# Performance work log

Hardware: AMD Instinct MI355X
Metric: run time of the kernel (lower is better)

The kernel has to match this reference:

```python
import jax, jax.numpy as jnp
import numpy as np

LMAX, MMAX = 4, 2
L1 = LMAX + 1                      # 5 coefficients with m=0
NL = [LMAX + 1 - m for m in range(MMAX + 1)]   # [5,4,3] degrees per |m|
K = (LMAX + 1) ** 2                # 25 full SH coefficients
KR = NL[0] + 2 * sum(NL[1:])       # 19 coefficients with |m|<=mmax
# degree l of each row in the reduced (m-primary) layout:
# m=0: l=0..4 | m=+1: l=1..4 | m=-1: l=1..4 | m=+2: l=2..4 | m=-2: l=2..4
L_IDX = np.array([0,1,2,3,4, 1,2,3,4, 1,2,3,4, 2,3,4, 2,3,4])


def so2_conv(x, rad, w0, b0, wr1, wi1, wr2, wi2, c_out, extra):
    """SO(2)-equivariant conv over m-primary layout x: [E, KR, c_in].
    rad: optional per-edge radial weights [E, sum_m nl_m*c_in]."""
    E, _, c_in = x.shape
    # m = 0 block
    x0 = x[:, :L1].reshape(E, L1 * c_in)
    if rad is not None:
        x0 = x0 * rad[:, :L1 * c_in]
    y0 = x0 @ w0 + b0
    out0 = y0[:, :L1 * c_out].reshape(E, L1, c_out)
    gating = y0[:, L1 * c_out:] if extra else None
    outs = [out0]
    off_x, off_r = L1, L1 * c_in
    for nl, wr, wi in ((NL[1], wr1, wi1), (NL[2], wr2, wi2)):
        xr = x[:, off_x:off_x + nl].reshape(E, nl * c_in)
        xi = x[:, off_x + nl:off_x + 2 * nl].reshape(E, nl * c_in)
        if rad is not None:
            rm = rad[:, off_r:off_r + nl * c_in]
            xr, xi = xr * rm, xi * rm
        yr = xr @ wr - xi @ wi   # complex-style SO2 mixing
        yi = xi @ wr + xr @ wi
        outs += [yr.reshape(E, nl, c_out), yi.reshape(E, nl, c_out)]
        off_x += 2 * nl
        off_r += nl * c_in
    return jnp.concatenate(outs, axis=1), gating


def gate_act(gating, x):
    """GateActivation: silu on l=0 scalars, sigmoid gates per degree l>=1."""
    E, _, H = x.shape
    g = jax.nn.sigmoid(gating).reshape(E, LMAX, H)
    g_ext = jnp.concatenate([jnp.ones((E, 1, H), x.dtype), g], axis=1)
    out = x * g_ext[:, L_IDX]           # l=0 row gated by 1, replaced below
    return out.at[:, 0].set(jax.nn.silu(x[:, 0]))


def setup_inputs() -> dict:
    key = jax.random.key(0)
    ks = jax.random.split(key, 32)
    E, N, C, H, D, RH = 50000, 2500, 64, 64, 128, 64
    c_in1 = 2 * C
    rad_dim = sum(nl * c_in1 for nl in NL)          # 1536
    extra = LMAX * H                                 # 256

    def w(k, shape):
        return jax.random.normal(k, shape, jnp.float32) / np.sqrt(shape[0])

    inp = {
        'node_feats': jax.random.normal(ks[0], (N, K, C), jnp.float32),
        'edge_embeds': jax.random.normal(ks[1], (E, D), jnp.float32),
        'wigner': jax.random.normal(ks[2], (E, KR, K), jnp.float32) / np.sqrt(K),
        'wigner_inv': jax.random.normal(ks[3], (E, K, KR), jnp.float32) / np.sqrt(KR),
        'edge_envelope': jax.random.uniform(ks[4], (E, 1, 1), jnp.float32),
        'rad_w1': w(ks[5], (D, RH)), 'rad_b1': jnp.zeros((RH,), jnp.float32),
        'rad_w2': w(ks[6], (RH, rad_dim)), 'rad_b2': jnp.zeros((rad_dim,), jnp.float32),
        'w1_m0': w(ks[7], (L1 * c_in1, L1 * H + extra)),
        'b1_m0': jnp.zeros((L1 * H + extra,), jnp.float32),
        'w1_r1': w(ks[8], (NL[1] * c_in1, NL[1] * H)),
        'w1_i1': w(ks[9], (NL[1] * c_in1, NL[1] * H)),
        'w1_r2': w(ks[10], (NL[2] * c_in1, NL[2] * H)),
        'w1_i2': w(ks[11], (NL[2] * c_in1, NL[2] * H)),
        'w2_m0': w(ks[12], (L1 * H, L1 * C)),
        'b2_m0': jnp.zeros((L1 * C,), jnp.float32),
        'w2_r1': w(ks[13], (NL[1] * H, NL[1] * C)),
        'w2_i1': w(ks[14], (NL[1] * H, NL[1] * C)),
        'w2_r2': w(ks[15], (NL[2] * H, NL[2] * C)),
        'w2_i2': w(ks[16], (NL[2] * H, NL[2] * C)),
        'senders': jax.random.randint(ks[17], (E,), 0, N, jnp.int32),
        'receivers': jax.random.randint(ks[18], (E,), 0, N, jnp.int32),
    }
    return inp


def reference(node_feats, edge_embeds, wigner, wigner_inv, edge_envelope,
              rad_w1, rad_b1, rad_w2, rad_b2,
              w1_m0, b1_m0, w1_r1, w1_i1, w1_r2, w1_i2,
              w2_m0, b2_m0, w2_r1, w2_i1, w2_r2, w2_i2,
              senders, receivers):
    num_nodes = node_feats.shape[0]
    C = node_feats.shape[2]
    H = w2_m0.shape[0] // L1
    # gather + concat: [E, K, 2C]
    msg = jnp.concatenate((node_feats[senders], node_feats[receivers]), axis=2)
    # rotate to edge frame, truncated to |m|<=mmax: [E, KR, 2C]
    msg = jnp.einsum('erk,ekc->erc', wigner, msg)
    # per-edge radial weights for conv1
    rad = jax.nn.silu(edge_embeds @ rad_w1 + rad_b1) @ rad_w2 + rad_b2
    msg, gating = so2_conv(msg, rad, w1_m0, b1_m0, w1_r1, w1_i1, w1_r2, w1_i2,
                           c_out=H, extra=LMAX * H)
    msg = gate_act(gating, msg)
    msg, _ = so2_conv(msg, None, w2_m0, b2_m0, w2_r1, w2_i1, w2_r2, w2_i2,
                      c_out=C, extra=0)
    msg = msg * edge_envelope
    # rotate back to global frame: [E, K, C]
    msg = jnp.einsum('ekr,erc->ekc', wigner_inv, msg)
    return jax.ops.segment_sum(msg, receivers, num_segments=num_nodes)
```

## Files before the change

### kernel.cpp

```cpp
#include <hip/hip_runtime.h>


typedef __attribute__((ext_vector_type(8))) short bf16x8;
typedef __attribute__((ext_vector_type(4))) float f32x4;

union U8 { uint4 v; unsigned short s[8]; };

__device__ __forceinline__ unsigned short f2b(float f) {
    unsigned u = __float_as_uint(f);
    unsigned r = (u + 0x7FFFu + ((u >> 16) & 1u)) >> 16;
    return (unsigned short)r;
}
__device__ __forceinline__ float b2f(unsigned short h) {
    return __uint_as_float(((unsigned)h) << 16);
}
__device__ __forceinline__ float sigm_(float x){ return 1.0f/(1.0f+__expf(-x)); }
__device__ __forceinline__ float silu_(float x){ return x/(1.0f+__expf(-x)); }

__device__ __forceinline__ void async16(short* lds, const short* g) {
    __builtin_amdgcn_global_load_lds(
        (const __attribute__((address_space(1))) void*)g,
        (__attribute__((address_space(3))) void*)lds, 16, 0, 0);
}

#define OFF_W1T   0L
#define OFF_W1C1  409600L
#define OFF_W1C2  933888L
#define OFF_V0T   1327104L
#define OFF_V1C   1449984L
#define OFF_V2C   1712128L
#define OFF_RW2T  1908736L
#define W_TOTAL   2007040L
#define NNODES    2500
#define NFT_ELEMS (2500L * 2048L)

__global__ void k_prep(const float* __restrict__ w1m0, const float* __restrict__ w1r1,
                       const float* __restrict__ w1i1, const float* __restrict__ w1r2,
                       const float* __restrict__ w1i2, const float* __restrict__ w2m0,
                       const float* __restrict__ w2r1, const float* __restrict__ w2i1,
                       const float* __restrict__ w2r2, const float* __restrict__ w2i2,
                       const float* __restrict__ rw2, short* __restrict__ W)
{
    long i = (long)blockIdx.x * blockDim.x + threadIdx.x;
    if (i >= W_TOTAL) return;
    float v;
    if (i < OFF_W1C1) {
        int n = (int)(i / 640), k = (int)(i % 640);
        v = (n < 576) ? w1m0[k * 576 + n] : 0.f;
    } else if (i < OFF_W1C2) {
        long j = i - OFF_W1C1; int n = (int)(j >> 10), k = (int)(j & 1023);
        v = (n < 256) ? ((k < 512) ? w1r1[k*256 + n] : -w1i1[(k-512)*256 + n])
                      : ((k < 512) ? w1i1[k*256 + (n-256)] : w1r1[(k-512)*256 + (n-256)]);
    } else if (i < OFF_V0T) {
        long j = i - OFF_W1C2; int n = (int)(j / 768), k = (int)(j % 768);
        v = (n >= 384) ? 0.f
          : (n < 192) ? ((k < 384) ? w1r2[k*192 + n] : -w1i2[(k-384)*192 + n])
                      : ((k < 384) ? w1i2[k*192 + (n-192)] : w1r2[(k-384)*192 + (n-192)]);
    } else if (i < OFF_V1C) {
        long j = i - OFF_V0T; int n = (int)(j / 320), k = (int)(j % 320);
        v = (n < 320) ? w2m0[k * 320 + n] : 0.f;
    } else if (i < OFF_V2C) {
        long j = i - OFF_V1C; int n = (int)(j >> 9), k = (int)(j & 511);
        v = (n < 256) ? ((k < 256) ? w2r1[k*256 + n] : -w2i1[(k-256)*256 + n])
                      : ((k < 256) ? w2i1[k*256 + (n-256)] : w2r1[(k-256)*256 + (n-256)]);
    } else if (i < OFF_RW2T) {
        long j = i - OFF_V2C; int n = (int)(j / 384), k = (int)(j % 384);
        v = (n >= 384) ? 0.f
          : (n < 192) ? ((k < 192) ? w2r2[k*192 + n] : -w2i2[(k-192)*192 + n])
                      : ((k < 192) ? w2i2[k*192 + (n-192)] : w2r2[(k-192)*192 + (n-192)]);
    } else {
        long j = i - OFF_RW2T; int n = (int)(j >> 6), d = (int)(j & 63);
        v = rw2[d * 1536 + n];
    }
    W[i] = (short)f2b(v);
}

__global__ __launch_bounds__(256)
void k_nft(const float* __restrict__ nf, short* __restrict__ nfT)
{
    __shared__ float s_nf[25 * 65];
    const int t = threadIdx.x;
    const long nn = blockIdx.x;
    for (int p = t; p < 1600; p += 256) {
        int r = p >> 6, c = p & 63;
        s_nf[r * 65 + c] = nf[nn * 1600 + p];
    }
    __syncthreads();
    for (int i = t; i < 2048; i += 256) {
        int c = i >> 5, k = i & 31;
        float v = (k < 25) ? s_nf[k * 65 + c] : 0.f;
        nfT[nn * 2048 + i] = (short)f2b(v);
    }
}

__global__ void k_hist(const int* __restrict__ rcv, int* __restrict__ cnt, long e0, long n)
{
    long e = (long)blockIdx.x * 256 + threadIdx.x;
    if (e < n) atomicAdd(&cnt[rcv[e0 + e]], 1);
}

__global__ __launch_bounds__(256)
void k_scan(const int* __restrict__ cnt, int* __restrict__ off, int* __restrict__ nxt)
{
    __shared__ int part[256];
    const int t = threadIdx.x;
    const int base = t * 10;
    int loc[10]; int s = 0;
    #pragma unroll
    for (int j = 0; j < 10; ++j) {
        int idx = base + j;
        int v = (idx < NNODES) ? cnt[idx] : 0;
        loc[j] = s; s += v;
    }
    part[t] = s;
    __syncthreads();
    for (int d = 1; d < 256; d <<= 1) {
        int v = part[t];
        int u = (t >= d) ? part[t - d] : 0;
        __syncthreads();
        part[t] = v + u;
        __syncthreads();
    }
    int excl = (t == 0) ? 0 : part[t - 1];
    #pragma unroll
    for (int j = 0; j < 10; ++j) {
        int idx = base + j;
        if (idx < NNODES) { int o = excl + loc[j]; off[idx] = o; nxt[idx] = o; }
    }
}

__global__ void k_scat(const int* __restrict__ rcv, int* __restrict__ nxt,
                       int* __restrict__ perm, long e0, long n)
{
    long e = (long)blockIdx.x * 256 + threadIdx.x;
    if (e < n) {
        int p = atomicAdd(&nxt[rcv[e0 + e]], 1);
        perm[p] = (int)e;
    }
}

__global__ __launch_bounds__(512)
void k_rad(const float* __restrict__ ee, const float* __restrict__ rw1,
           const float* __restrict__ rb1, const float* __restrict__ rb2,
           const short* __restrict__ RW2T, short* __restrict__ rad,
           long e0, long Etot)
{
    __shared__ __align__(16) short s_h[32 * 64];
    const int t = threadIdx.x, w = t >> 6, l = t & 63, l15 = l & 15, lhi = l >> 4;
    const long eb = (long)blockIdx.x * 32;

    #pragma unroll
    for (int j = 0; j < 4; ++j) {
        int i = t + j * 512;
        int e = i >> 6, d = i & 63;
        long ge = e0 + eb + e;
        float a = rb1[d];
        if (ge < Etot) {
            const float* ep = ee + ge * 128;
            #pragma unroll 16
            for (int dd = 0; dd < 128; ++dd) a = fmaf(ep[dd], rw1[dd * 64 + d], a);
            a = silu_(a);
        } else a = 0.f;
        *(short*)((char*)s_h + e * 128 + ((d * 2) ^ ((e & 7) << 4))) = (short)f2b(a);
    }
    __syncthreads();

    f32x4 acc[6][2][2];
    #pragma unroll
    for (int g = 0; g < 6; ++g)
        #pragma unroll
        for (int mt = 0; mt < 2; ++mt)
            #pragma unroll
            for (int nt = 0; nt < 2; ++nt)
                acc[g][mt][nt] = (f32x4){0.f, 0.f, 0.f, 0.f};

    #pragma unroll
    for (int ks = 0; ks < 2; ++ks) {
        bf16x8 af[2];
        #pragma unroll
        for (int mt = 0; mt < 2; ++mt)
            af[mt] = *(const bf16x8*)((const char*)s_h + (mt * 16 + l15) * 128 +
                                      (((ks << 6) + (lhi << 4)) ^ ((l & 7) << 4)));
        #pragma unroll
        for (int g = 0; g < 6; ++g) {
            int grp = w + g * 8;
            #pragma unroll
            for (int nt = 0; nt < 2; ++nt) {
                int col = grp * 32 + nt * 16 + l15;
                bf16x8 bf = *(const bf16x8*)(RW2T + (long)col * 64 + (ks << 5) + (lhi << 3));
                #pragma unroll
                for (int mt = 0; mt < 2; ++mt)
                    acc[g][mt][nt] = __builtin_amdgcn_mfma_f32_16x16x32_bf16(af[mt], bf, acc[g][mt][nt], 0, 0, 0);
            }
        }
    }
    #pragma unroll
    for (int g = 0; g < 6; ++g)
        #pragma unroll
        for (int nt = 0; nt < 2; ++nt) {
            int col = (w + g * 8) * 32 + nt * 16 + l15;
            float bias = rb2[col];
            #pragma unroll
            for (int mt = 0; mt < 2; ++mt)
                #pragma unroll
                for (int r = 0; r < 4; ++r) {
                    int e = mt * 16 + lhi * 4 + r;
                    rad[(eb + e) * 1536 + col] = (short)f2b(acc[g][mt][nt][r] + bias);
                }
        }
}

__global__ __launch_bounds__(256)
void k_rot2(const float* __restrict__ wig, const short* __restrict__ nfT,
            const short* __restrict__ rad,
            const int* __restrict__ snd, const int* __restrict__ rcv,
            short* __restrict__ X, long e0, long nchunk)
{
    __shared__ float s_wg[4][480];
    __shared__ __align__(16) short s_rot[4][20 * 128];
    const int t = threadIdx.x, w = t >> 6, l = t & 63, l15 = l & 15, lhi = l >> 4;
    const long eb = (long)blockIdx.x * 4;
    const long el = eb + w;
    const bool valid = (el < nchunk);

    for (int p = t; p < 4 * 475; p += 256) {
        int e = p / 475, q = p - e * 475;
        if (eb + e < nchunk) s_wg[e][q] = wig[(e0 + eb + e) * 475 + q];
    }
    __syncthreads();

    if (valid) {
        long ge = e0 + el;
        int n0 = snd[ge], n1 = rcv[ge];
        U8 a0u, a1u;
        #pragma unroll
        for (int j = 0; j < 8; ++j) {
            int k = lhi * 8 + j;
            a0u.s[j] = (k < 25) ? f2b(s_wg[w][l15 * 25 + k]) : (unsigned short)0;
            a1u.s[j] = (l15 < 3 && k < 25) ? f2b(s_wg[w][(16 + l15) * 25 + k]) : (unsigned short)0;
        }
        bf16x8 a0 = *(bf16x8*)&a0u, a1 = *(bf16x8*)&a1u;

        f32x4 acc0[8], acc1[8];
        #pragma unroll
        for (int nt = 0; nt < 8; ++nt) {
            acc0[nt] = (f32x4){0.f, 0.f, 0.f, 0.f};
            acc1[nt] = (f32x4){0.f, 0.f, 0.f, 0.f};
        }
        #pragma unroll
        for (int nt = 0; nt < 8; ++nt) {
            int col = nt * 16 + l15;
            bf16x8 b = *(const bf16x8*)(nfT + (long)(col < 64 ? n0 : n1) * 2048 +
                                        (long)(col & 63) * 32 + (lhi << 3));
            acc0[nt] = __builtin_amdgcn_mfma_f32_16x16x32_bf16(a0, b, acc0[nt], 0, 0, 0);
            acc1[nt] = __builtin_amdgcn_mfma_f32_16x16x32_bf16(a1, b, acc1[nt], 0, 0, 0);
        }
        char* base = (char*)s_rot[w];
        #pragma unroll
        for (int nt = 0; nt < 8; ++nt) {
            int col2 = (nt * 16 + l15) * 2;
            #pragma unroll
            for (int r = 0; r < 4; ++r) {
                int row = lhi * 4 + r;
                *(short*)(base + ((row * 256 + col2) ^ ((row & 7) << 4))) = (short)f2b(acc0[nt][r]);
            }
            if (lhi == 0) {
                #pragma unroll
                for (int r = 0; r < 4; ++r) {
                    int row = 16 + r;
                    *(short*)(base + ((row * 256 + col2) ^ ((row & 7) << 4))) = (short)f2b(acc1[nt][r]);
                }
            }
        }
    }
    __syncthreads();

    short* xp = X + el * 2432;
    if (valid) {
        const short* rp = rad + el * 1536;
        #pragma unroll
        for (int it = 0; it < 5; ++it) {
            int q = l + it * 64;
            if (q < 304) {
                int r = q >> 4, c0 = (q & 15) << 3;
                int rr = (r < 9) ? r : ((r < 16) ? r - 4 : r - 7);
                U8 rot; rot.v = *(uint4*)((char*)s_rot[w] + ((r * 256 + c0 * 2) ^ ((r & 7) << 4)));
                U8 rd;  rd.v  = *(const uint4*)(rp + rr * 128 + c0);
                U8 o;
                #pragma unroll
                for (int j = 0; j < 8; ++j) o.s[j] = f2b(b2f(rot.s[j]) * b2f(rd.s[j]));
                *(uint4*)(xp + q * 8) = o.v;
            }
        }
    } else {
        #pragma unroll
        for (int it = 0; it < 5; ++it) {
            int q = l + it * 64;
            if (q < 304) *(uint4*)(xp + q * 8) = (uint4){0, 0, 0, 0};
        }
    }
}

__global__ __launch_bounds__(256)
void k_gate(short* __restrict__ Zr, long nitems)
{
    long idx = (long)blockIdx.x * 256 + threadIdx.x;
    if (idx >= nitems) return;
    long e = idx / 152;
    int jg = (int)(idx - e * 152);
    int j = jg * 8;
    short* rp = Zr + e * 1536;
    U8 z; z.v = *(const uint4*)(rp + j);
    U8 o;
    if (j < 320) {
        int rr = j >> 6;
        if (rr == 0) {
            #pragma unroll
            for (int q = 0; q < 8; ++q) o.s[q] = f2b(silu_(b2f(z.s[q])));
        } else {
            U8 g; g.v = *(const uint4*)(rp + 1216 + (rr - 1) * 64 + (j & 63));
            #pragma unroll
            for (int q = 0; q < 8; ++q) o.s[q] = f2b(b2f(z.s[q]) * b2f(g.s[q]));
        }
    } else if (j < 832) {
        U8 g; g.v = *(const uint4*)(rp + 1216 + ((j - 320) & 255));
        #pragma unroll
        for (int q = 0; q < 8; ++q) o.s[q] = f2b(b2f(z.s[q]) * b2f(g.s[q]));
    } else {
        int gi = j - 832; if (gi >= 192) gi -= 192;
        U8 g; g.v = *(const uint4*)(rp + 1280 + gi);
        #pragma unroll
        for (int q = 0; q < 8; ++q) o.s[q] = f2b(b2f(z.s[q]) * b2f(g.s[q]));
    }
    *(uint4*)(rp + j) = o.v;
}

template<int Km, int Nreal, int EPI>
__device__ __forceinline__ void gemm_body(
    const short* __restrict__ A, const long RS,
    const short* __restrict__ W, const float* __restrict__ bias,
    short* __restrict__ O, const long OS, const int oofs,
    short* __restrict__ sA, short* __restrict__ sB, const int et, const int cb)
{
    const int t = threadIdx.x, w = t >> 6, l = t & 63, l15 = l & 15, lhi = l >> 4;
    const int wm = w & 1, wn = w >> 1;
    const long eb = (long)et * 128;
    const short* Ap = A + eb * RS;
    const short* Wp = W + (long)cb * Km;

    f32x4 acc[4][4];
    #pragma unroll
    for (int mt = 0; mt < 4; ++mt)
        #pragma unroll
        for (int nt = 0; nt < 4; ++nt)
            acc[mt][nt] = (f32x4){0.f, 0.f, 0.f, 0.f};

    int rowA[2], k8A[2];
    #pragma unroll
    for (int i = 0; i < 2; ++i) {
        int s = i * 512 + t;
        rowA[i] = s >> 3;
        k8A[i]  = (s & 7) ^ (rowA[i] & 7);
    }
    int rowB[4], k8B[4];
    #pragma unroll
    for (int i = 0; i < 4; ++i) {
        int s = i * 512 + t;
        rowB[i] = s >> 3;
        k8B[i]  = (s & 7) ^ (rowB[i] & 7);
    }
    const int wb = w << 6;

    const int rx = l & 7;
    constexpr int NCH = Km / 64;
    for (int ch = 0; ch < NCH; ++ch) {
        const int kc = ch * 64;
        __syncthreads();
        #pragma unroll
        for (int i = 0; i < 2; ++i)
            async16(sA + (i * 512 + wb) * 8, Ap + (long)rowA[i] * RS + kc + k8A[i] * 8);
        #pragma unroll
        for (int i = 0; i < 4; ++i)
            async16(sB + (i * 512 + wb) * 8, Wp + (long)rowB[i] * Km + kc + k8B[i] * 8);
        __syncthreads();
        #pragma unroll
        for (int ks = 0; ks < 2; ++ks) {
            const int ko = (((ks << 2) + lhi) ^ rx) << 3;
            bf16x8 af[4], bf[4];
            #pragma unroll
            for (int mt = 0; mt < 4; ++mt) {
                int row = wm * 64 + mt * 16 + l15;
                af[mt] = *(const bf16x8*)(sA + row * 64 + ko);
            }
            #pragma unroll
            for (int nt = 0; nt < 4; ++nt) {
                int row = wn * 64 + nt * 16 + l15;
                bf[nt] = *(const bf16x8*)(sB + row * 64 + ko);
            }
            #pragma unroll
            for (int mt = 0; mt < 4; ++mt)
                #pragma unroll
                for (int nt = 0; nt < 4; ++nt)
                    acc[mt][nt] = __builtin_amdgcn_mfma_f32_16x16x32_bf16(af[mt], bf[nt], acc[mt][nt], 0, 0, 0);
        }
    }

    const int r0 = wm * 64, c0 = wn * 64;
    #pragma unroll
    for (int nt = 0; nt < 4; ++nt) {
        int jj = cb + c0 + nt * 16 + l15;
        if (jj < Nreal) {
            float b = (EPI >= 1) ? bias[jj] : 0.f;
            #pragma unroll
            for (int mt = 0; mt < 4; ++mt)
                #pragma unroll
                for (int r = 0; r < 4; ++r) {
                    long e = eb + r0 + mt * 16 + lhi * 4 + r;
                    float v = acc[mt][nt][r] + b;
                    if constexpr (EPI == 2) {
                        if (jj < 320) O[e * OS + jj] = (short)f2b(v);
                        else          O[e * OS + 1216 + (jj - 320)] = (short)f2b(sigm_(v));
                    } else {
                        O[e * OS + oofs + jj] = (short)f2b(v);
                    }
                }
        }
    }
}

__global__ __launch_bounds__(512)
void k_conv1(const short* __restrict__ X, const short* __restrict__ W0,
             const short* __restrict__ W1, const short* __restrict__ W2,
             const float* __restrict__ b1m0, short* __restrict__ Zr, int nbt)
{
    __shared__ __align__(16) short sA[8192];
    __shared__ __align__(16) short sB[16384];
    const int bid = blockIdx.x;
    const int s = bid >> 3;
    const int et = (bid & 7) + ((s / 7) << 3);
    const int ph = s % 7;
    if (et >= nbt) return;
    if (ph < 3)
        gemm_body< 640, 576, 2>(X,        2432, W0, b1m0,   Zr, 1536, 0,   sA, sB, et, ph << 8);
    else if (ph < 5)
        gemm_body<1024, 512, 0>(X + 640,  2432, W1, nullptr, Zr, 1536, 320, sA, sB, et, (ph - 3) << 8);
    else
        gemm_body< 768, 384, 0>(X + 1664, 2432, W2, nullptr, Zr, 1536, 832, sA, sB, et, (ph - 5) << 8);
}

__global__ __launch_bounds__(512)
void k_conv2(const short* __restrict__ Zr, const short* __restrict__ V0,
             const short* __restrict__ V1, const short* __restrict__ V2,
             const float* __restrict__ b2m0, short* __restrict__ Y2, int nbt)
{
    __shared__ __align__(16) short sA[8192];
    __shared__ __align__(16) short sB[16384];
    const int bid = blockIdx.x;
    const int s = bid >> 3;
    const int et = (bid & 7) + ((s / 6) << 3);
    const int ph = s % 6;
    if (et >= nbt) return;
    if (ph < 2)
        gemm_body<320, 320, 1>(Zr,       1536, V0, b2m0,   Y2, 1216, 0,   sA, sB, et, ph << 8);
    else if (ph < 4)
        gemm_body<512, 512, 0>(Zr + 320, 1536, V1, nullptr, Y2, 1216, 320, sA, sB, et, (ph - 2) << 8);
    else
        gemm_body<384, 384, 0>(Zr + 832, 1536, V2, nullptr, Y2, 1216, 832, sA, sB, et, (ph - 4) << 8);
}

__global__ __launch_bounds__(256)
void k_invn(const short* __restrict__ Y2, const float* __restrict__ winv,
            const float* __restrict__ env, const int* __restrict__ cnt,
            const int* __restrict__ off, const int* __restrict__ perm,
            float* __restrict__ out, long e0)
{
    __shared__ __align__(16) short s_y[2][1216];
    __shared__ float s_wv[2][476];
    const int t = threadIdx.x;
    const int n = blockIdx.x;
    const int deg = cnt[n], start = off[n];

    float acc[7];
    #pragma unroll
    for (int j = 0; j < 7; ++j) acc[j] = 0.f;

    auto stage = [&](int i, int b) {
        int el = perm[start + i];
        long ge = e0 + el;
        if (t < 152) ((uint4*)s_y[b])[t] = *(const uint4*)(Y2 + (long)el * 1216 + t * 8);
        for (int p = t; p < 475; p += 256) s_wv[b][p] = winv[ge * 475 + p];
        if (t == 0) s_wv[b][475] = env[ge];
    };

    if (deg > 0) stage(0, 0);
    for (int i = 0; i < deg; ++i) {
        __syncthreads();
        if (i + 1 < deg) stage(i + 1, (i + 1) & 1);
        const short* sy = s_y[i & 1];
        const float* sw = s_wv[i & 1];
        float ev = sw[475];
        #pragma unroll
        for (int j = 0; j < 7; ++j) {
            int f = t + j * 256;
            if (f < 1600) {
                int r = f >> 6, c = f & 63;
                float a = 0.f;
                #pragma unroll
                for (int k = 0; k < 19; ++k)
                    a = fmaf(sw[r * 19 + k], b2f((unsigned short)sy[k * 64 + c]), a);
                acc[j] = fmaf(a, ev, acc[j]);
            }
        }
    }
    #pragma unroll
    for (int j = 0; j < 7; ++j) {
        int f = t + j * 256;
        if (f < 1600) out[(long)n * 1600 + f] += acc[j];
    }
}

extern "C" void kernel_launch(void* const* d_in, const int* in_sizes, int n_in,
                              void* d_out, int out_size, void* d_ws, size_t ws_size,
                              hipStream_t stream)
{
    const float* nf   = (const float*)d_in[0];
    const float* ee   = (const float*)d_in[1];
    const float* wig  = (const float*)d_in[2];
    const float* winv = (const float*)d_in[3];
    const float* env  = (const float*)d_in[4];
    const float* rw1  = (const float*)d_in[5];
    const float* rb1  = (const float*)d_in[6];
    const float* rw2  = (const float*)d_in[7];
    const float* rb2  = (const float*)d_in[8];
    const float* w1m0 = (const float*)d_in[9];
    const float* b1m0 = (const float*)d_in[10];
    const float* w1r1 = (const float*)d_in[11];
    const float* w1i1 = (const float*)d_in[12];
    const float* w1r2 = (const float*)d_in[13];
    const float* w1i2 = (const float*)d_in[14];
    const float* w2m0 = (const float*)d_in[15];
    const float* b2m0 = (const float*)d_in[16];
    const float* w2r1 = (const float*)d_in[17];
    const float* w2i1 = (const float*)d_in[18];
    const float* w2r2 = (const float*)d_in[19];
    const float* w2i2 = (const float*)d_in[20];
    const int*   snd  = (const int*)d_in[21];
    const int*   rcv  = (const int*)d_in[22];
    float* out = (float*)d_out;

    const long E = in_sizes[21];

    short* Wb  = (short*)d_ws;
    short* nfT = Wb + W_TOTAL;
    int* cnt   = (int*)(nfT + NFT_ELEMS);
    int* off   = cnt + 2512;
    int* nxt   = off + 2512;
    int* perm  = nxt + 2512;

    const size_t fixed = (size_t)W_TOTAL * 2 + (size_t)NFT_ELEMS * 2 + 3 * 2512 * 4;
    long cap = (ws_size > fixed) ? (long)((ws_size - fixed) / 7940) : 128;
    long chunk = (cap / 128) * 128;
    if (chunk < 128) chunk = 128;
    long Epad = ((E + 127) / 128) * 128;
    if (chunk > Epad) chunk = Epad;

    short* Xc = (short*)(perm + chunk);
    short* Rc = Xc + chunk * 2432;

    hipMemsetAsync(d_out, 0, (size_t)out_size * sizeof(float), stream);
    k_prep<<<(int)((W_TOTAL + 511) / 512), 512, 0, stream>>>(
        w1m0, w1r1, w1i1, w1r2, w1i2, w2m0, w2r1, w2i1, w2r2, w2i2, rw2, Wb);
    k_nft<<<NNODES, 256, 0, stream>>>(nf, nfT);

    for (long base = 0; base < E; base += chunk) {
        long n = E - base; if (n > chunk) n = chunk;
        int nb2 = (int)((n + 127) / 128);
        int nb8 = ((nb2 + 7) / 8) * 8;
        int nbe = (int)((n + 255) / 256);

        hipMemsetAsync(cnt, 0, NNODES * sizeof(int), stream);
        k_hist<<<nbe, 256, 0, stream>>>(rcv, cnt, base, n);
        k_scan<<<1, 256, 0, stream>>>(cnt, off, nxt);
        k_scat<<<nbe, 256, 0, stream>>>(rcv, nxt, perm, base, n);

        k_rad <<<(int)((n + 31) / 32), 512, 0, stream>>>(ee, rw1, rb1, rb2, Wb + OFF_RW2T, Rc, base, E);
        k_rot2<<<nb2 * 32, 256, 0, stream>>>(wig, nfT, Rc, snd, rcv, Xc, base, n);

        k_conv1<<<nb8 * 7, 512, 0, stream>>>(Xc, Wb + OFF_W1T, Wb + OFF_W1C1, Wb + OFF_W1C2, b1m0, Rc, nb2);

        long nitems = (long)nb2 * 128 * 152;
        k_gate<<<(int)((nitems + 255) / 256), 256, 0, stream>>>(Rc, nitems);

        k_conv2<<<nb8 * 6, 512, 0, stream>>>(Rc, Wb + OFF_V0T, Wb + OFF_V1C, Wb + OFF_V2C, b2m0, Xc, nb2);

        k_invn<<<NNODES, 256, 0, stream>>>(Xc, winv, env, cnt, off, perm, out, base);
    }
    (void)n_in;
}
```

Before: 1.034 ms.

## Double-buffer GEMM LDS tiles with 32-wide K chunks and prefetch

The shared GEMM body now splits K into 32-element chunks and keeps two LDS buffers. It issues the async global-to-LDS loads for the next chunk before running the MFMAs on the current one, with one barrier per iteration instead of two. The goal is to overlap the tile loads with compute while keeping the same total LDS footprint. The cost is twice as many loop iterations and barriers, and a narrower 4-way XOR swizzle on 64-byte rows that may raise LDS bank conflicts.

```diff
diff --git a/kernel.cpp b/kernel.cpp
--- a/kernel.cpp
+++ b/kernel.cpp
@@ -355,54 +355,53 @@
         for (int nt = 0; nt < 4; ++nt)
             acc[mt][nt] = (f32x4){0.f, 0.f, 0.f, 0.f};
 
-    int rowA[2], k8A[2];
+    const int rowA0 = t >> 2, k8A0 = (t & 3) ^ (rowA0 & 3);
+    int rowB[2], k8B[2];
     #pragma unroll
     for (int i = 0; i < 2; ++i) {
         int s = i * 512 + t;
-        rowA[i] = s >> 3;
-        k8A[i]  = (s & 7) ^ (rowA[i] & 7);
-    }
-    int rowB[4], k8B[4];
-    #pragma unroll
-    for (int i = 0; i < 4; ++i) {
-        int s = i * 512 + t;
-        rowB[i] = s >> 3;
-        k8B[i]  = (s & 7) ^ (rowB[i] & 7);
+        rowB[i] = s >> 2;
+        k8B[i]  = (s & 3) ^ (rowB[i] & 3);
     }
     const int wb = w << 6;
 
-    const int rx = l & 7;
-    constexpr int NCH = Km / 64;
+    auto stage = [&](int buf, int kc) {
+        short* dA = sA + buf * 4096;
+        short* dB = sB + buf * 8192;
+        async16(dA + wb * 8, Ap + (long)rowA0 * RS + kc + k8A0 * 8);
+        #pragma unroll
+        for (int i = 0; i < 2; ++i)
+            async16(dB + (i * 512 + wb) * 8, Wp + (long)rowB[i] * Km + kc + k8B[i] * 8);
+    };
+
+    const int rx = l15 & 3;
+    constexpr int NCH = Km / 32;
+    stage(0, 0);
+    __syncthreads();
+    int cur = 0;
     for (int ch = 0; ch < NCH; ++ch) {
-        const int kc = ch * 64;
+        if (ch + 1 < NCH) stage(cur ^ 1, (ch + 1) * 32);
+        const short* bA = sA + cur * 4096;
+        const short* bB = sB + cur * 8192;
+        const int ko = (lhi ^ rx) << 3;
+        bf16x8 af[4], bf[4];
+        #pragma unroll
+        for (int mt = 0; mt < 4; ++mt) {
+            int row = wm * 64 + mt * 16 + l15;
+            af[mt] = *(const bf16x8*)(bA + row * 32 + ko);
+        }
+        #pragma unroll
+        for (int nt = 0; nt < 4; ++nt) {
+            int row = wn * 64 + nt * 16 + l15;
+            bf[nt] = *(const bf16x8*)(bB + row * 32 + ko);
+        }
+        #pragma unroll
+        for (int mt = 0; mt < 4; ++mt)
+            #pragma unroll
+            for (int nt = 0; nt < 4; ++nt)
+                acc[mt][nt] = __builtin_amdgcn_mfma_f32_16x16x32_bf16(af[mt], bf[nt], acc[mt][nt], 0, 0, 0);
         __syncthreads();
-        #pragma unroll
-        for (int i = 0; i < 2; ++i)
-            async16(sA + (i * 512 + wb) * 8, Ap + (long)rowA[i] * RS + kc + k8A[i] * 8);
-        #pragma unroll
-        for (int i = 0; i < 4; ++i)
-            async16(sB + (i * 512 + wb) * 8, Wp + (long)rowB[i] * Km + kc + k8B[i] * 8);
-        __syncthreads();
-        #pragma unroll
-        for (int ks = 0; ks < 2; ++ks) {
-            const int ko = (((ks << 2) + lhi) ^ rx) << 3;
-            bf16x8 af[4], bf[4];
-            #pragma unroll
-            for (int mt = 0; mt < 4; ++mt) {
-                int row = wm * 64 + mt * 16 + l15;
-                af[mt] = *(const bf16x8*)(sA + row * 64 + ko);
-            }
-            #pragma unroll
-            for (int nt = 0; nt < 4; ++nt) {
-                int row = wn * 64 + nt * 16 + l15;
-                bf[nt] = *(const bf16x8*)(sB + row * 64 + ko);
-            }
-            #pragma unroll
-            for (int mt = 0; mt < 4; ++mt)
-                #pragma unroll
-                for (int nt = 0; nt < 4; ++nt)
-                    acc[mt][nt] = __builtin_amdgcn_mfma_f32_16x16x32_bf16(af[mt], bf[nt], acc[mt][nt], 0, 0, 0);
-        }
+        cur ^= 1;
     }
 
     const int r0 = wm * 64, c0 = wn * 64;
@@ -433,8 +432,8 @@
              const short* __restrict__ W1, const short* __restrict__ W2,
              const float* __restrict__ b1m0, short* __restrict__ Zr, int nbt)
 {
-    __shared__ __align__(16) short sA[8192];
-    __shared__ __align__(16) short sB[16384];
+    __shared__ __align__(16) short sA[2 * 4096];
+    __shared__ __align__(16) short sB[2 * 8192];
     const int bid = blockIdx.x;
     const int s = bid >> 3;
     const int et = (bid & 7) + ((s / 7) << 3);
@@ -453,8 +452,8 @@
              const short* __restrict__ V1, const short* __restrict__ V2,
              const float* __restrict__ b2m0, short* __restrict__ Y2, int nbt)
 {
-    __shared__ __align__(16) short sA[8192];
-    __shared__ __align__(16) short sB[16384];
+    __shared__ __align__(16) short sA[2 * 4096];
+    __shared__ __align__(16) short sB[2 * 8192];
     const int bid = blockIdx.x;
     const int s = bid >> 3;
     const int et = (bid & 7) + ((s / 6) << 3);
```

New measurement: 1.083 ms. 4.7% more time.
